# Optimization experiments

Hardware: AMD Instinct MI355X
Metric: run time of the kernel (lower is better)

The kernel has to match this reference:

```python
import jax, jax.numpy as jnp
import numpy as np
from jax import lax

K_, B_, C_, H_, W_ = 7, 4, 64, 96, 96
HEAD = 256
HM_C, BZ_C, ID_C, WH_C = 24, 16, 128, 14


def conv2d(x, w, b, pad):
    y = lax.conv_general_dilated(x, w, (1, 1), [(pad, pad), (pad, pad)],
                                 dimension_numbers=('NCHW', 'OIHW', 'NCHW'))
    return y + b[None, :, None, None]


def deform_conv2d(x, off_w, off_b, w, b, G, kh=3, kw=3, pad=1):
    """Modulated deformable conv (DCNv2), stride=1, dilation=1.
    Offset/mask come from a regular conv on x (conv_offset_mask), chunked into
    (y-offsets, x-offsets, mask) along channels as in the DCNv2 reference.
    """
    B, Cin, H, W = x.shape
    Cg = Cin // G
    KK = kh * kw
    om = conv2d(x, off_w, off_b, pad)              # [B, 3*G*KK, H, W]
    om = om.reshape(B, 3, G, KK, H, W)             # torch.chunk(out, 3, dim=1)
    off_y, off_x = om[:, 0], om[:, 1]              # [B,G,KK,H,W]
    mask = jax.nn.sigmoid(om[:, 2])                # [B,G,KK,H,W]
    ky, kx = jnp.meshgrid(jnp.arange(kh), jnp.arange(kw), indexing='ij')
    base_y = (jnp.arange(H)[None, :, None] - pad + ky.reshape(KK)[:, None, None]).astype(x.dtype)
    base_x = (jnp.arange(W)[None, None, :] - pad + kx.reshape(KK)[:, None, None]).astype(x.dtype)
    sy = base_y[None, None] + off_y                # sampling y coords [B,G,KK,H,W]
    sx = base_x[None, None] + off_x
    y0f = jnp.floor(sy); x0f = jnp.floor(sx)
    wy = sy - y0f; wx = sx - x0f
    y0 = y0f.astype(jnp.int32); x0 = x0f.astype(jnp.int32)
    xg = x.reshape(B, G, Cg, H * W)

    def gather(yc, xc, wgt):
        valid = ((yc >= 0) & (yc < H) & (xc >= 0) & (xc < W)).astype(x.dtype)
        idx = (jnp.clip(yc, 0, H - 1) * W + jnp.clip(xc, 0, W - 1)).reshape(B, G, 1, KK * H * W)
        v = jnp.take_along_axis(xg, idx, axis=3).reshape(B, G, Cg, KK, H, W)
        return v * (wgt * valid)[:, :, None]

    cols = (gather(y0, x0, (1 - wy) * (1 - wx)) + gather(y0, x0 + 1, (1 - wy) * wx)
            + gather(y0 + 1, x0, wy * (1 - wx)) + gather(y0 + 1, x0 + 1, wy * wx))
    cols = cols * mask[:, :, None]                 # modulation, [B,G,Cg,KK,H,W]
    Cout = w.shape[0]
    out = jnp.einsum('bgckhw,ogck->bohw', cols, w.reshape(Cout, G, Cg, KK))
    return out + b[None, :, None, None]


def setup_inputs() -> dict:
    key = jax.random.key(0)
    ks = jax.random.split(key, 16)
    G, KK = K_, 9

    def w(k, shape, s=0.02):
        return jax.random.normal(k, shape, jnp.float32) * s

    return {
        'features': jax.random.normal(ks[0], (K_, B_, C_, H_, W_), jnp.float32),
        'hm_w1': w(ks[1], (HEAD, C_, 3, 3)), 'hm_b1': jnp.zeros((HEAD,), jnp.float32),
        'hm_w2': w(ks[2], (HM_C, HEAD, 1, 1)), 'hm_b2': jnp.full((HM_C,), -2.19, jnp.float32),
        'wh_w1': w(ks[3], (HEAD, C_, 3, 3)), 'wh_b1': jnp.zeros((HEAD,), jnp.float32),
        'wh_w2': w(ks[4], (WH_C // K_, HEAD, 1, 1)), 'wh_b2': jnp.zeros((WH_C // K_,), jnp.float32),
        'id_w1': w(ks[5], (HEAD, K_ * C_, 3, 3)), 'id_b1': jnp.zeros((HEAD,), jnp.float32),
        'id_w2': w(ks[6], (ID_C, HEAD, 1, 1)), 'id_b2': jnp.zeros((ID_C,), jnp.float32),
        'off_w': w(ks[7], (3 * G * KK, K_ * C_, 3, 3), 0.003), 'off_b': jnp.zeros((3 * G * KK,), jnp.float32),
        'dcn_w': w(ks[8], (HEAD, K_ * C_, 3, 3)), 'dcn_b': jnp.zeros((HEAD,), jnp.float32),
        'bn_gamma': jnp.ones((HEAD,), jnp.float32), 'bn_beta': jnp.zeros((HEAD,), jnp.float32),
        'bn_mean': jnp.zeros((HEAD,), jnp.float32), 'bn_var': jnp.ones((HEAD,), jnp.float32),
        'bz_w': w(ks[9], (BZ_C, HEAD, 1, 1)), 'bz_b': jnp.zeros((BZ_C,), jnp.float32),
    }


def reference(features, hm_w1, hm_b1, hm_w2, hm_b2, wh_w1, wh_b1, wh_w2, wh_b2,
              id_w1, id_b1, id_w2, id_b2, off_w, off_b, dcn_w, dcn_b,
              bn_gamma, bn_beta, bn_mean, bn_var, bz_w, bz_b):
    K, B, C, H, W = features.shape
    # wh branch applied to every frame, concatenated k-major along channels
    f = features.reshape(K * B, C, H, W)
    owh = conv2d(jax.nn.relu(conv2d(f, wh_w1, wh_b1, 1)), wh_w2, wh_b2, 0)
    c = owh.shape[1]
    owh = owh.reshape(K, B, c, H, W).transpose(1, 0, 2, 3, 4).reshape(B, K * c, H, W)
    # hm branch on middle frame (K//2)
    hm = conv2d(jax.nn.relu(conv2d(features[K // 2], hm_w1, hm_b1, 1)), hm_w2, hm_b2, 0)
    # torch.cat(input_chunk, dim=1)
    cat = features.transpose(1, 0, 2, 3, 4).reshape(B, K * C, H, W)
    idout = conv2d(jax.nn.relu(conv2d(cat, id_w1, id_b1, 1)), id_w2, id_b2, 0)
    # bezier_ctp branch: DCN -> BN (inference stats) -> ReLU -> 1x1 conv
    d = deform_conv2d(cat, off_w, off_b, dcn_w, dcn_b, G=K)
    scale = (bn_gamma * lax.rsqrt(bn_var + 1e-5))[None, :, None, None]
    d = (d - bn_mean[None, :, None, None]) * scale + bn_beta[None, :, None, None]
    bz = conv2d(jax.nn.relu(d), bz_w, bz_b, 0)
    return hm, bz, idout, owh
```

## Files before the change

### kernel.cpp

```cpp
#include <hip/hip_runtime.h>
#include <hip/hip_bf16.h>
#include <math.h>

#define KF   7
#define BB_  4
#define CC_  64
#define HH   96
#define WW   96
#define HWSZ 9216
#define HEAD 256
#define CH2  448

typedef __bf16 bf16x8 __attribute__((ext_vector_type(8)));
typedef __bf16 bf16x4 __attribute__((ext_vector_type(4)));
typedef float  f32x4  __attribute__((ext_vector_type(4)));
typedef float  f32x2  __attribute__((ext_vector_type(2)));
typedef unsigned int u32;

__device__ __forceinline__ f32x2 pkmul(f32x2 a, f32x2 b) {
    f32x2 d; asm("v_pk_mul_f32 %0, %1, %2" : "=v"(d) : "v"(a), "v"(b)); return d;
}
__device__ __forceinline__ f32x2 pkfma(f32x2 a, f32x2 b, f32x2 c) {
    f32x2 d; asm("v_pk_fma_f32 %0, %1, %2, %3" : "=v"(d) : "v"(a), "v"(b), "v"(c)); return d;
}
__device__ __forceinline__ u32 cvtpk_bf16(f32x2 a) {
    u32 d; asm("v_cvt_pk_bf16_f32 %0, %1, %2" : "=v"(d) : "v"(a[0]), "v"(a[1])); return d;
}
__device__ __forceinline__ f32x2 unpk_bf16x2(u32 v) {
    f32x2 r;
    r[0] = __uint_as_float(v << 16);
    r[1] = __uint_as_float(v & 0xffff0000u);
    return r;
}

__device__ __forceinline__ void taps_body(const float* __restrict__ w,
                                          __bf16* __restrict__ out,
                                          int Cout, int Cin, int CoutPad, int e) {
    int tot = Cout * Cin * 9;
    if (e >= tot) return;
    int co = e / (Cin * 9);
    int r  = e - co * (Cin * 9);
    int ci = r / 9;
    int k  = r - ci * 9;
    int kc = ci >> 5, cw = ci & 31;
    out[(((size_t)k * (Cin >> 5) + kc) * CoutPad + co) * 32 + cw] = (__bf16)w[e];
}

__global__ __launch_bounds__(256) void prep_all(
    const float* __restrict__ feat, __bf16* __restrict__ X2,
    const float* __restrict__ wh_w1, __bf16* __restrict__ wh_wT2,
    const float* __restrict__ hm_w1, __bf16* __restrict__ hm_wT2,
    const float* __restrict__ id_w1, __bf16* __restrict__ id_wT2,
    const float* __restrict__ off_w, __bf16* __restrict__ off_wT2,
    const float* __restrict__ wh_w2, __bf16* __restrict__ wh_w2b,
    const float* __restrict__ hm_w2, __bf16* __restrict__ hm_w2b,
    const float* __restrict__ id_w2, __bf16* __restrict__ id_w2b,
    const float* __restrict__ bz_w,  __bf16* __restrict__ bz_wb,
    const float* __restrict__ dcn_w, __bf16* __restrict__ dcn_wA)
{
    __shared__ float sT[96][65];
    const int bid = blockIdx.x;
    const int t   = threadIdx.x;

    if (bid < 2688) {
        const int h = bid % 96;
        const int n = bid / 96;
        const int g = n >> 2, b = n & 3;
        const float* src = feat + (size_t)n * 64 * HWSZ + h * WW;
        for (int e = t; e < 6144; e += 256) {
            int c = e / 96, w = e - c * 96;
            sT[w][c] = src[(size_t)c * HWSZ + w];
        }
        __syncthreads();
        for (int u = t; u < 768; u += 256) {
            int w = u >> 3, c8 = (u & 7) * 8;
            __bf16 tmp[8];
#pragma unroll
            for (int i = 0; i < 8; ++i) tmp[i] = (__bf16)sT[w][c8 + i];
            *(uint4*)&X2[(((size_t)(b * 96 + h)) * 96 + w) * CH2 + g * 64 + c8] =
                *(const uint4*)tmp;
        }
        return;
    }

    if (bid < 3264) { taps_body(wh_w1, wh_wT2, 256, 64, 256, (bid - 2688) * 256 + t); return; }
    if (bid < 3840) { taps_body(hm_w1, hm_wT2, 256, 64, 256, (bid - 3264) * 256 + t); return; }
    if (bid < 7872) { taps_body(id_w1, id_wT2, 256, 448, 256, (bid - 3840) * 256 + t); return; }
    if (bid < 10849){ taps_body(off_w, off_wT2, 189, 448, 256, (bid - 7872) * 256 + t); return; }
    if (bid < 10851){ int e = (bid - 10849) * 256 + t; if (e < 512)   wh_w2b[e] = (__bf16)wh_w2[e]; return; }
    if (bid < 10875){ int e = (bid - 10851) * 256 + t; if (e < 6144)  hm_w2b[e] = (__bf16)hm_w2[e]; return; }
    if (bid < 11003){ int e = (bid - 10875) * 256 + t; if (e < 32768) id_w2b[e] = (__bf16)id_w2[e]; return; }
    if (bid < 11019){ int e = (bid - 11003) * 256 + t; if (e < 4096)  bz_wb[e]  = (__bf16)bz_w[e];  return; }
    {
        int e = (bid - 11019) * 256 + t;
        if (e >= 256 * 4032) return;
        int co = e / 4032;
        int r  = e - co * 4032;
        int g  = r / 576;
        int r2 = r - g * 576;
        int tap = r2 >> 6;
        int c   = r2 & 63;
        dcn_wA[((size_t)(r >> 5) * 256 + co) * 32 + (r & 31)] =
            (__bf16)dcn_w[((size_t)co * 448 + g * 64 + c) * 9 + tap];
    }
}

template<int MPW, int MODE>
__device__ __forceinline__ void conv_body(
    char* smem,
    const __bf16* __restrict__ X2,
    const __bf16* __restrict__ wT2,
    const float* __restrict__ b1,
    const __bf16* __restrict__ w2b,
    const float* __restrict__ b2,
    float* __restrict__ out,
    int Cin, int CmidPad, int Cf, int chanBase, int whMap,
    int h, int img)
{
    __bf16 (*sX)[3][98][40] = (__bf16 (*)[3][98][40])smem;

    const int t    = threadIdx.x;
    const int wave = t >> 6;
    const int lane = t & 63;
    const int lq   = lane >> 4;
    const int lr   = lane & 15;
    const int mbase = wave * (MPW * 16);

    const int bImg = whMap ? (img & 3) : img;
    const int cb   = whMap ? ((img >> 2) * 64) : chanBase;
    const __bf16* Xrow = X2 + ((size_t)bImg * 96) * 96 * CH2;

    const bool doGemm = (MODE != 2) || (mbase < Cf);

    f32x4 acc[MPW][6];
#pragma unroll
    for (int mi = 0; mi < MPW; ++mi)
#pragma unroll
        for (int ni = 0; ni < 6; ++ni)
            acc[mi][ni] = (f32x4){0.f, 0.f, 0.f, 0.f};

    const int KC = Cin >> 5;

    for (int u = t; u < 1176; u += 512) {
        int pos = u >> 2;
        int q   = u & 3;
        int r   = pos / 98;
        int gw  = pos - r * 98;
        int gh  = h - 1 + r;
        int gx  = gw - 1;
        uint4 v = {0u, 0u, 0u, 0u};
        if (((unsigned)gh < 96u) && ((unsigned)gx < 96u))
            v = *(const uint4*)&Xrow[((size_t)gh * 96 + gx) * CH2 + cb + q * 8];
        *(uint4*)&sX[0][r][gw][q * 8] = v;
    }
    __syncthreads();

    for (int kc = 0; kc < KC; ++kc) {
        uint4 pv[3];
        if (kc + 1 < KC) {
#pragma unroll
            for (int i = 0; i < 3; ++i) {
                int u = t + i * 512;
                uint4 v = {0u, 0u, 0u, 0u};
                if (u < 1176) {
                    int pos = u >> 2;
                    int q   = u & 3;
                    int r   = pos / 98;
                    int gw  = pos - r * 98;
                    int gh  = h - 1 + r;
                    int gx  = gw - 1;
                    if (((unsigned)gh < 96u) && ((unsigned)gx < 96u))
                        v = *(const uint4*)&Xrow[((size_t)gh * 96 + gx) * CH2 +
                                                 cb + (kc + 1) * 32 + q * 8];
                }
                pv[i] = v;
            }
        }
        asm volatile("" ::: "memory");

        const int buf = kc & 1;
        if (doGemm) {
            const __bf16* wkc = wT2 + ((size_t)kc * CmidPad + mbase + lr) * 32 + lq * 8;
            const size_t tapStride = (size_t)KC * CmidPad * 32;
#pragma unroll
            for (int tap = 0; tap < 9; ++tap) {
                const int ky = tap / 3, kx = tap - ky * 3;
                const __bf16* wt = wkc + (size_t)tap * tapStride;
                bf16x8 aF[MPW];
#pragma unroll
                for (int mi = 0; mi < MPW; ++mi)
                    aF[mi] = *(const bf16x8*)(wt + mi * 512);
#pragma unroll
                for (int ni = 0; ni < 6; ++ni) {
                    bf16x8 bF = *(const bf16x8*)&sX[buf][ky][ni * 16 + lr + kx][lq * 8];
#pragma unroll
                    for (int mi = 0; mi < MPW; ++mi)
                        acc[mi][ni] = __builtin_amdgcn_mfma_f32_16x16x32_bf16(
                            aF[mi], bF, acc[mi][ni], 0, 0, 0);
                }
            }
        }

        if (kc + 1 < KC) {
#pragma unroll
            for (int i = 0; i < 3; ++i) {
                int u = t + i * 512;
                if (u < 1176) {
                    int pos = u >> 2;
                    int q   = u & 3;
                    int r   = pos / 98;
                    int gw  = pos - r * 98;
                    *(uint4*)&sX[buf ^ 1][r][gw][q * 8] = pv[i];
                }
            }
        }
        __syncthreads();
    }

    if (MODE == 2) {
#pragma unroll
        for (int mi = 0; mi < MPW; ++mi)
#pragma unroll
            for (int ni = 0; ni < 6; ++ni) {
                int px = ni * 16 + lr;
#pragma unroll
                for (int r = 0; r < 4; ++r) {
                    int co = mbase + mi * 16 + lq * 4 + r;
                    if (co < Cf)
                        out[((size_t)(img * 189 + co)) * HWSZ + h * WW + px] =
                            acc[mi][ni][r] + b1[co];
                }
            }
        return;
    } else {
        __syncthreads();
        __bf16 (*sH)[264] = (__bf16 (*)[264])smem;
#pragma unroll
        for (int mi = 0; mi < MPW; ++mi) {
            int co0 = mbase + mi * 16 + lq * 4;
            float bb0 = b1[co0], bb1 = b1[co0 + 1], bb2 = b1[co0 + 2], bb3 = b1[co0 + 3];
#pragma unroll
            for (int ni = 0; ni < 6; ++ni) {
                int px = ni * 16 + lr;
                bf16x4 hv;
                hv[0] = (__bf16)fmaxf(acc[mi][ni][0] + bb0, 0.f);
                hv[1] = (__bf16)fmaxf(acc[mi][ni][1] + bb1, 0.f);
                hv[2] = (__bf16)fmaxf(acc[mi][ni][2] + bb2, 0.f);
                hv[3] = (__bf16)fmaxf(acc[mi][ni][3] + bb3, 0.f);
                *(bf16x4*)&sH[px][co0] = hv;
            }
        }
        __syncthreads();

        const int MT2 = (Cf + 15) >> 4;
        for (int tt = wave; tt < MT2 * 6; tt += 8) {
            int ni = tt / MT2;
            int mt = tt - ni * MT2;
            int cf = mt * 16 + lr; if (cf > Cf - 1) cf = Cf - 1;
            const __bf16* wrow = w2b + (size_t)cf * 256 + lq * 8;
            f32x4 c = (f32x4){0.f, 0.f, 0.f, 0.f};
#pragma unroll
            for (int kc = 0; kc < 8; ++kc) {
                bf16x8 aF = *(const bf16x8*)(wrow + kc * 32);
                bf16x8 bF = *(const bf16x8*)&sH[ni * 16 + lr][kc * 32 + lq * 8];
                c = __builtin_amdgcn_mfma_f32_16x16x32_bf16(aF, bF, c, 0, 0, 0);
            }
            int px = ni * 16 + lr;
#pragma unroll
            for (int r = 0; r < 4; ++r) {
                int cfr = mt * 16 + lq * 4 + r;
                if (cfr < Cf) {
                    int och;
                    if (MODE == 1) {
                        och = (img & 3) * 14 + (img >> 2) * 2 + cfr;
                    } else {
                        och = img * Cf + cfr;
                    }
                    out[(size_t)och * HWSZ + h * WW + px] = c[r] + b2[cfr];
                }
            }
        }
    }
}

__global__ __launch_bounds__(512, 4) void conv_all(
    const __bf16* __restrict__ X2,
    const __bf16* __restrict__ idT, const float* __restrict__ id_b1,
    const __bf16* __restrict__ id_w2b, const float* __restrict__ id_b2,
    float* __restrict__ out_id,
    const __bf16* __restrict__ offT, const float* __restrict__ off_b,
    float* __restrict__ off_out,
    const __bf16* __restrict__ whT, const float* __restrict__ wh_b1,
    const __bf16* __restrict__ wh_w2b, const float* __restrict__ wh_b2,
    float* __restrict__ out_wh,
    const __bf16* __restrict__ hmT, const float* __restrict__ hm_b1,
    const __bf16* __restrict__ hm_w2b, const float* __restrict__ hm_b2,
    float* __restrict__ out_hm)
{
    __shared__ __align__(16) char smem[50688];
    const int h = blockIdx.x;
    const int y = blockIdx.y;
    if (y < 4)
        conv_body<2, 0>(smem, X2, idT, id_b1, id_w2b, id_b2, out_id,
                        448, 256, 128, 0, 0, h, y);
    else if (y < 8)
        conv_body<2, 2>(smem, X2, offT, off_b, nullptr, nullptr, off_out,
                        448, 256, 189, 0, 0, h, y - 4);
    else if (y < 36)
        conv_body<2, 1>(smem, X2, whT, wh_b1, wh_w2b, wh_b2, out_wh,
                        64, 256, 2, 0, 1, h, y - 8);
    else
        conv_body<2, 0>(smem, X2, hmT, hm_b1, hm_w2b, hm_b2, out_hm,
                        64, 256, 24, 192, 0, h, y - 36);
}

#define DNP 48
__global__ __launch_bounds__(512) void dcn_bz_mfma(
    const __bf16* __restrict__ X2,
    const float* __restrict__ offmap,
    const __bf16* __restrict__ wA,
    const float* __restrict__ dcn_b,
    const float* __restrict__ bn_g, const float* __restrict__ bn_be,
    const float* __restrict__ bn_mn, const float* __restrict__ bn_vr,
    const __bf16* __restrict__ bzwb,
    const float* __restrict__ bzb,
    float* __restrict__ out_bz)
{
    __shared__ __align__(16) char smem[33600];
    __bf16 (*sC)[DNP][40] = (__bf16 (*)[DNP][40])smem;
    __bf16 (*sD)[DNP][40] = (__bf16 (*)[DNP][40])smem;
    float4* sW4   = (float4*)(smem + 30720);
    int*    sWoff = (int*)  (smem + 30720 + 2304);

    const int fid = blockIdx.x + blockIdx.y * 192;
    const int nf  = (fid & 7) * 96 + (fid >> 3);
    const int b   = nf / 192;
    const int r_  = nf - b * 192;
    const int h   = r_ >> 1;
    const int w0  = (r_ & 1) * DNP;

    const int t    = threadIdx.x;
    const int wave = t >> 6;
    const int lane = t & 63;
    const int lq   = lane >> 4;
    const int lr   = lane & 15;
    const int mbase = wave * 32;
    const int grp  = t >> 3;
    const int lsub = t & 7;

    const float* offp = offmap + (size_t)b * 189 * HWSZ;
    const __bf16* Xb  = X2 + ((size_t)b * 96) * 96 * CH2;

    f32x4 acc[2][3];
#pragma unroll
    for (int mi = 0; mi < 2; ++mi)
#pragma unroll
        for (int ni = 0; ni < 3; ++ni)
            acc[mi][ni] = (f32x4){0.f, 0.f, 0.f, 0.f};

    for (int g = 0; g < KF; ++g) {
        for (int c3 = 0; c3 < 3; ++c3) {
            __syncthreads();
            if (t < 144) {
                int tl = t / 48;
                int px = t - tl * 48;
                int pix = h * WW + w0 + px;
                int gk  = g * 9 + c3 * 3 + tl;
                float oy = offp[(size_t)gk * HWSZ + pix];
                float ox = offp[(size_t)(63 + gk) * HWSZ + pix];
                float mv = offp[(size_t)(126 + gk) * HWSZ + pix];
                float m  = 1.f / (1.f + expf(-mv));
                float sy = (float)(h - 1 + c3) + oy;
                float sx = (float)(w0 + px - 1 + tl) + ox;
                float fy = floorf(sy), fx = floorf(sx);
                float wy = sy - fy,    wx = sx - fx;
                int y0 = (int)fy, x0 = (int)fx;
                int by = min(max(y0, 0), 94);
                int bx = min(max(x0, 0), 94);
                float wy0 = (y0 == by ? 1.f - wy : 0.f) + (y0 + 1 == by ? wy : 0.f);
                float wy1 = (y0 == by + 1 ? 1.f - wy : 0.f) + (y0 + 1 == by + 1 ? wy : 0.f);
                float wx0 = (x0 == bx ? 1.f - wx : 0.f) + (x0 + 1 == bx ? wx : 0.f);
                float wx1 = (x0 == bx + 1 ? 1.f - wx : 0.f) + (x0 + 1 == bx + 1 ? wx : 0.f);
                float4 wv;
                wv.x = m * wy0 * wx0; wv.y = m * wy0 * wx1;
                wv.z = m * wy1 * wx0; wv.w = m * wy1 * wx1;
                sW4[t]   = wv;
                sWoff[t] = by * 96 + bx;
            }
            __syncthreads();
            for (int p = grp; p < 144; p += 64) {
                float4 wv = sW4[p];
                int base  = sWoff[p];
                int tl = p / 48;
                int px = p - tl * 48;
                const __bf16* pl = Xb + (size_t)base * CH2 + g * 64 + lsub * 8;
                bf16x8 c00 = *(const bf16x8*)(pl);
                bf16x8 c01 = *(const bf16x8*)(pl + CH2);
                bf16x8 c10 = *(const bf16x8*)(pl + 96 * CH2);
                bf16x8 c11 = *(const bf16x8*)(pl + 97 * CH2);
                f32x2 vw00 = {wv.x, wv.x}, vw01 = {wv.y, wv.y};
                f32x2 vw10 = {wv.z, wv.z}, vw11 = {wv.w, wv.w};
                const u32* p00 = (const u32*)&c00;
                const u32* p01 = (const u32*)&c01;
                const u32* p10 = (const u32*)&c10;
                const u32* p11 = (const u32*)&c11;
                u32 o[4];
#pragma unroll
                for (int pp = 0; pp < 4; ++pp) {
                    f32x2 a = pkmul(vw00, unpk_bf16x2(p00[pp]));
                    a = pkfma(vw01, unpk_bf16x2(p01[pp]), a);
                    a = pkfma(vw10, unpk_bf16x2(p10[pp]), a);
                    a = pkfma(vw11, unpk_bf16x2(p11[pp]), a);
                    o[pp] = cvtpk_bf16(a);
                }
                int kc = tl * 2 + (lsub >> 2);
                *(uint4*)&sC[kc][px][(lsub & 3) * 8] = *(const uint4*)o;
            }
            __syncthreads();
            const __bf16* wbase = wA + ((size_t)(g * 18 + c3 * 6) * 256 +
                                        mbase + lr) * 32 + lq * 8;
#pragma unroll
            for (int kc = 0; kc < 6; ++kc) {
                const __bf16* wk = wbase + (size_t)kc * 256 * 32;
                bf16x8 aF[2];
#pragma unroll
                for (int mi = 0; mi < 2; ++mi)
                    aF[mi] = *(const bf16x8*)(wk + mi * 512);
#pragma unroll
                for (int ni = 0; ni < 3; ++ni) {
                    bf16x8 bF = *(const bf16x8*)&sC[kc][ni * 16 + lr][lq * 8];
#pragma unroll
                    for (int mi = 0; mi < 2; ++mi)
                        acc[mi][ni] = __builtin_amdgcn_mfma_f32_16x16x32_bf16(
                            aF[mi], bF, acc[mi][ni], 0, 0, 0);
                }
            }
        }
    }

    __syncthreads();
#pragma unroll
    for (int mi = 0; mi < 2; ++mi) {
        int co0 = mbase + mi * 16 + lq * 4;
        float sc[4], sh[4];
#pragma unroll
        for (int r = 0; r < 4; ++r) {
            float s = bn_g[co0 + r] * rsqrtf(bn_vr[co0 + r] + 1e-5f);
            sc[r] = s;
            sh[r] = (dcn_b[co0 + r] - bn_mn[co0 + r]) * s + bn_be[co0 + r];
        }
#pragma unroll
        for (int ni = 0; ni < 3; ++ni) {
            int px = ni * 16 + lr;
            bf16x4 hv;
#pragma unroll
            for (int r = 0; r < 4; ++r)
                hv[r] = (__bf16)fmaxf(acc[mi][ni][r] * sc[r] + sh[r], 0.f);
            *(bf16x4*)&sD[co0 >> 5][px][co0 & 31] = hv;
        }
    }
    __syncthreads();

    if (wave < 3) {
        int ni = wave;
        const __bf16* wrow = bzwb + (size_t)lr * 256 + lq * 8;
        f32x4 c = (f32x4){0.f, 0.f, 0.f, 0.f};
#pragma unroll
        for (int kc = 0; kc < 8; ++kc) {
            bf16x8 aF = *(const bf16x8*)(wrow + kc * 32);
            bf16x8 bF = *(const bf16x8*)&sD[kc][ni * 16 + lr][lq * 8];
            c = __builtin_amdgcn_mfma_f32_16x16x32_bf16(aF, bF, c, 0, 0, 0);
        }
        int px = ni * 16 + lr;
#pragma unroll
        for (int r = 0; r < 4; ++r) {
            int cf = lq * 4 + r;
            out_bz[((size_t)(b * 16 + cf)) * HWSZ + h * WW + w0 + px] = c[r] + bzb[cf];
        }
    }
}

extern "C" void kernel_launch(void* const* d_in, const int* in_sizes, int n_in,
                              void* d_out, int out_size, void* d_ws, size_t ws_size,
                              hipStream_t stream) {
    const float* feat   = (const float*)d_in[0];
    const float* hm_w1  = (const float*)d_in[1];
    const float* hm_b1  = (const float*)d_in[2];
    const float* hm_w2  = (const float*)d_in[3];
    const float* hm_b2  = (const float*)d_in[4];
    const float* wh_w1  = (const float*)d_in[5];
    const float* wh_b1  = (const float*)d_in[6];
    const float* wh_w2  = (const float*)d_in[7];
    const float* wh_b2  = (const float*)d_in[8];
    const float* id_w1  = (const float*)d_in[9];
    const float* id_b1  = (const float*)d_in[10];
    const float* id_w2  = (const float*)d_in[11];
    const float* id_b2  = (const float*)d_in[12];
    const float* off_w  = (const float*)d_in[13];
    const float* off_b  = (const float*)d_in[14];
    const float* dcn_w  = (const float*)d_in[15];
    const float* dcn_b  = (const float*)d_in[16];
    const float* bn_g   = (const float*)d_in[17];
    const float* bn_be  = (const float*)d_in[18];
    const float* bn_mn  = (const float*)d_in[19];
    const float* bn_vr  = (const float*)d_in[20];
    const float* bz_w   = (const float*)d_in[21];
    const float* bz_b   = (const float*)d_in[22];

    float* ws      = (float*)d_ws;
    float* off_out = ws;
    __bf16* X2     = (__bf16*)(off_out + 6967296);
    __bf16* bfw    = X2 + 16515072;
    __bf16* wh_wT2 = bfw;
    __bf16* hm_wT2 = wh_wT2 + 147456;
    __bf16* id_wT2 = hm_wT2 + 147456;
    __bf16* off_wT2= id_wT2 + 1032192;
    __bf16* wh_w2b = off_wT2 + 1032192;
    __bf16* hm_w2b = wh_w2b + 512;
    __bf16* id_w2b = hm_w2b + 6144;
    __bf16* dcn_wA = id_w2b + 32768;
    __bf16* bz_wb  = dcn_wA + 1032192;

    float* out_hm = (float*)d_out;
    float* out_bz = out_hm + 884736;
    float* out_id = out_bz + 589824;
    float* out_wh = out_id + 4718592;

    prep_all<<<15051, 256, 0, stream>>>(
        feat, X2,
        wh_w1, wh_wT2, hm_w1, hm_wT2, id_w1, id_wT2, off_w, off_wT2,
        wh_w2, wh_w2b, hm_w2, hm_w2b, id_w2, id_w2b, bz_w, bz_wb,
        dcn_w, dcn_wA);

    conv_all<<<dim3(96, 40), 512, 0, stream>>>(
        X2,
        id_wT2, id_b1, id_w2b, id_b2, out_id,
        off_wT2, off_b, off_out,
        wh_wT2, wh_b1, wh_w2b, wh_b2, out_wh,
        hm_wT2, hm_b1, hm_w2b, hm_b2, out_hm);

    dcn_bz_mfma<<<dim3(192, 4), 512, 0, stream>>>(
        X2, off_out, dcn_wA, dcn_b, bn_g, bn_be, bn_mn, bn_vr,
        bz_wb, bz_b, out_bz);
}
```

Measured before the change: 565.9 us.

## Software-pipeline DCN gather, sampling-weight and MFMA phases with double buffering

Splits the DCN loop body into three phases: sampling-weight computation, bilinear gather into LDS, and the MFMA accumulation. It runs them as a software pipeline over the 21 (group, row) stages, with double-buffered LDS for the weights and the gathered columns. This cuts the barriers per stage from three to one and lets the global gather loads overlap the MFMA work of the previous stage. In exchange, LDS use per block rises to about 52 KB, and a min-occupancy launch bound is added that may force register limits or spills.

```diff
diff --git a/kernel.cpp b/kernel.cpp
--- a/kernel.cpp
+++ b/kernel.cpp
@@ -315,7 +315,7 @@
 }
 
 #define DNP 48
-__global__ __launch_bounds__(512) void dcn_bz_mfma(
+__global__ __launch_bounds__(512, 6) void dcn_bz_mfma(
     const __bf16* __restrict__ X2,
     const float* __restrict__ offmap,
     const __bf16* __restrict__ wA,
@@ -326,11 +326,11 @@
     const float* __restrict__ bzb,
     float* __restrict__ out_bz)
 {
-    __shared__ __align__(16) char smem[33600];
-    __bf16 (*sC)[DNP][40] = (__bf16 (*)[DNP][40])smem;
-    __bf16 (*sD)[DNP][40] = (__bf16 (*)[DNP][40])smem;
-    float4* sW4   = (float4*)(smem + 30720);
-    int*    sWoff = (int*)  (smem + 30720 + 2304);
+    __shared__ __align__(16) char smem[51840];
+    __bf16 (*sC)[6][DNP][40] = (__bf16 (*)[6][DNP][40])smem;
+    __bf16 (*sD)[DNP][40]    = (__bf16 (*)[DNP][40])smem;
+    float4 (*sW4)[144] = (float4 (*)[144])(smem + 46080);
+    int    (*sWo)[144] = (int    (*)[144])(smem + 46080 + 4608);
 
     const int fid = blockIdx.x + blockIdx.y * 192;
     const int nf  = (fid & 7) * 96 + (fid >> 3);
@@ -358,87 +358,104 @@
         for (int ni = 0; ni < 3; ++ni)
             acc[mi][ni] = (f32x4){0.f, 0.f, 0.f, 0.f};
 
-    for (int g = 0; g < KF; ++g) {
-        for (int c3 = 0; c3 < 3; ++c3) {
-            __syncthreads();
-            if (t < 144) {
-                int tl = t / 48;
-                int px = t - tl * 48;
-                int pix = h * WW + w0 + px;
-                int gk  = g * 9 + c3 * 3 + tl;
-                float oy = offp[(size_t)gk * HWSZ + pix];
-                float ox = offp[(size_t)(63 + gk) * HWSZ + pix];
-                float mv = offp[(size_t)(126 + gk) * HWSZ + pix];
-                float m  = 1.f / (1.f + expf(-mv));
-                float sy = (float)(h - 1 + c3) + oy;
-                float sx = (float)(w0 + px - 1 + tl) + ox;
-                float fy = floorf(sy), fx = floorf(sx);
-                float wy = sy - fy,    wx = sx - fx;
-                int y0 = (int)fy, x0 = (int)fx;
-                int by = min(max(y0, 0), 94);
-                int bx = min(max(x0, 0), 94);
-                float wy0 = (y0 == by ? 1.f - wy : 0.f) + (y0 + 1 == by ? wy : 0.f);
-                float wy1 = (y0 == by + 1 ? 1.f - wy : 0.f) + (y0 + 1 == by + 1 ? wy : 0.f);
-                float wx0 = (x0 == bx ? 1.f - wx : 0.f) + (x0 + 1 == bx ? wx : 0.f);
-                float wx1 = (x0 == bx + 1 ? 1.f - wx : 0.f) + (x0 + 1 == bx + 1 ? wx : 0.f);
-                float4 wv;
-                wv.x = m * wy0 * wx0; wv.y = m * wy0 * wx1;
-                wv.z = m * wy1 * wx0; wv.w = m * wy1 * wx1;
-                sW4[t]   = wv;
-                sWoff[t] = by * 96 + bx;
-            }
-            __syncthreads();
-            for (int p = grp; p < 144; p += 64) {
-                float4 wv = sW4[p];
-                int base  = sWoff[p];
-                int tl = p / 48;
-                int px = p - tl * 48;
-                const __bf16* pl = Xb + (size_t)base * CH2 + g * 64 + lsub * 8;
-                bf16x8 c00 = *(const bf16x8*)(pl);
-                bf16x8 c01 = *(const bf16x8*)(pl + CH2);
-                bf16x8 c10 = *(const bf16x8*)(pl + 96 * CH2);
-                bf16x8 c11 = *(const bf16x8*)(pl + 97 * CH2);
-                f32x2 vw00 = {wv.x, wv.x}, vw01 = {wv.y, wv.y};
-                f32x2 vw10 = {wv.z, wv.z}, vw11 = {wv.w, wv.w};
-                const u32* p00 = (const u32*)&c00;
-                const u32* p01 = (const u32*)&c01;
-                const u32* p10 = (const u32*)&c10;
-                const u32* p11 = (const u32*)&c11;
-                u32 o[4];
-#pragma unroll
-                for (int pp = 0; pp < 4; ++pp) {
-                    f32x2 a = pkmul(vw00, unpk_bf16x2(p00[pp]));
-                    a = pkfma(vw01, unpk_bf16x2(p01[pp]), a);
-                    a = pkfma(vw10, unpk_bf16x2(p10[pp]), a);
-                    a = pkfma(vw11, unpk_bf16x2(p11[pp]), a);
-                    o[pp] = cvtpk_bf16(a);
-                }
-                int kc = tl * 2 + (lsub >> 2);
-                *(uint4*)&sC[kc][px][(lsub & 3) * 8] = *(const uint4*)o;
-            }
-            __syncthreads();
-            const __bf16* wbase = wA + ((size_t)(g * 18 + c3 * 6) * 256 +
-                                        mbase + lr) * 32 + lq * 8;
-#pragma unroll
-            for (int kc = 0; kc < 6; ++kc) {
-                const __bf16* wk = wbase + (size_t)kc * 256 * 32;
-                bf16x8 aF[2];
+    auto Aph = [&](int cc, int sel) {
+        if (t < 144) {
+            int tl = t / 48;
+            int px = t - tl * 48;
+            int pix = h * WW + w0 + px;
+            int g = cc / 3, c3 = cc - g * 3;
+            int gk  = g * 9 + c3 * 3 + tl;
+            float oy = offp[(size_t)gk * HWSZ + pix];
+            float ox = offp[(size_t)(63 + gk) * HWSZ + pix];
+            float mv = offp[(size_t)(126 + gk) * HWSZ + pix];
+            float m  = 1.f / (1.f + expf(-mv));
+            float sy = (float)(h - 1 + c3) + oy;
+            float sx = (float)(w0 + px - 1 + tl) + ox;
+            float fy = floorf(sy), fx = floorf(sx);
+            float wy = sy - fy,    wx = sx - fx;
+            int y0 = (int)fy, x0 = (int)fx;
+            int by = min(max(y0, 0), 94);
+            int bx = min(max(x0, 0), 94);
+            float wy0 = (y0 == by ? 1.f - wy : 0.f) + (y0 + 1 == by ? wy : 0.f);
+            float wy1 = (y0 == by + 1 ? 1.f - wy : 0.f) + (y0 + 1 == by + 1 ? wy : 0.f);
+            float wx0 = (x0 == bx ? 1.f - wx : 0.f) + (x0 + 1 == bx ? wx : 0.f);
+            float wx1 = (x0 == bx + 1 ? 1.f - wx : 0.f) + (x0 + 1 == bx + 1 ? wx : 0.f);
+            float4 wv;
+            wv.x = m * wy0 * wx0; wv.y = m * wy0 * wx1;
+            wv.z = m * wy1 * wx0; wv.w = m * wy1 * wx1;
+            sW4[sel][t] = wv;
+            sWo[sel][t] = by * 96 + bx;
+        }
+    };
+
+    auto Bph = [&](int cc, int sel) {
+        const int g = cc / 3;
+        for (int p = grp; p < 144; p += 64) {
+            float4 wv = sW4[sel][p];
+            int base  = sWo[sel][p];
+            int tl = p / 48;
+            int px = p - tl * 48;
+            const __bf16* pl = Xb + (size_t)base * CH2 + g * 64 + lsub * 8;
+            bf16x8 c00 = *(const bf16x8*)(pl);
+            bf16x8 c01 = *(const bf16x8*)(pl + CH2);
+            bf16x8 c10 = *(const bf16x8*)(pl + 96 * CH2);
+            bf16x8 c11 = *(const bf16x8*)(pl + 97 * CH2);
+            f32x2 vw00 = {wv.x, wv.x}, vw01 = {wv.y, wv.y};
+            f32x2 vw10 = {wv.z, wv.z}, vw11 = {wv.w, wv.w};
+            const u32* p00 = (const u32*)&c00;
+            const u32* p01 = (const u32*)&c01;
+            const u32* p10 = (const u32*)&c10;
+            const u32* p11 = (const u32*)&c11;
+            u32 o[4];
+#pragma unroll
+            for (int pp = 0; pp < 4; ++pp) {
+                f32x2 a = pkmul(vw00, unpk_bf16x2(p00[pp]));
+                a = pkfma(vw01, unpk_bf16x2(p01[pp]), a);
+                a = pkfma(vw10, unpk_bf16x2(p10[pp]), a);
+                a = pkfma(vw11, unpk_bf16x2(p11[pp]), a);
+                o[pp] = cvtpk_bf16(a);
+            }
+            int kc = tl * 2 + (lsub >> 2);
+            *(uint4*)&sC[sel][kc][px][(lsub & 3) * 8] = *(const uint4*)o;
+        }
+    };
+
+    auto Cph = [&](int cc, int sel) {
+        const int g  = cc / 3;
+        const int c3 = cc - g * 3;
+        const __bf16* wbase = wA + ((size_t)(g * 18 + c3 * 6) * 256 +
+                                    mbase + lr) * 32 + lq * 8;
+#pragma unroll
+        for (int kc = 0; kc < 6; ++kc) {
+            const __bf16* wk = wbase + (size_t)kc * 256 * 32;
+            bf16x8 aF[2];
+#pragma unroll
+            for (int mi = 0; mi < 2; ++mi)
+                aF[mi] = *(const bf16x8*)(wk + mi * 512);
+#pragma unroll
+            for (int ni = 0; ni < 3; ++ni) {
+                bf16x8 bF = *(const bf16x8*)&sC[sel][kc][ni * 16 + lr][lq * 8];
 #pragma unroll
                 for (int mi = 0; mi < 2; ++mi)
-                    aF[mi] = *(const bf16x8*)(wk + mi * 512);
-#pragma unroll
-                for (int ni = 0; ni < 3; ++ni) {
-                    bf16x8 bF = *(const bf16x8*)&sC[kc][ni * 16 + lr][lq * 8];
-#pragma unroll
-                    for (int mi = 0; mi < 2; ++mi)
-                        acc[mi][ni] = __builtin_amdgcn_mfma_f32_16x16x32_bf16(
-                            aF[mi], bF, acc[mi][ni], 0, 0, 0);
-                }
-            }
-        }
-    }
-
+                    acc[mi][ni] = __builtin_amdgcn_mfma_f32_16x16x32_bf16(
+                        aF[mi], bF, acc[mi][ni], 0, 0, 0);
+            }
+        }
+    };
+
+    Aph(0, 0);
     __syncthreads();
+    Bph(0, 0);
+    Aph(1, 1);
+    __syncthreads();
+
+    for (int cc = 0; cc < 21; ++cc) {
+        if (cc + 1 < 21) Bph(cc + 1, (cc + 1) & 1);
+        if (cc + 2 < 21) Aph(cc + 2, cc & 1);
+        Cph(cc, cc & 1);
+        __syncthreads();
+    }
+
 #pragma unroll
     for (int mi = 0; mi < 2; ++mi) {
         int co0 = mbase + mi * 16 + lq * 4;
```

After: 510.9 us, median of 2. -9.7%, faster.
